# Optimization experiments

Measured on AMD Instinct MI355X. Metric: run time of the kernel, lower is better.

## Reference

```python
import jax, jax.numpy as jnp
import numpy as np

EPS = 1e-12  # matches torch F.normalize default eps

def _l2_normalize(x):
    # F.normalize: x / max(||x||, eps)
    n = jnp.linalg.norm(x, axis=-1, keepdims=True)
    return x / jnp.maximum(n, EPS)

def setup_inputs() -> dict:
    key = jax.random.key(0)
    k1, k2 = jax.random.split(key)
    sat = jax.random.normal(k1, (256, 64, 128), dtype=jnp.float32)   # [b, j, d]
    pano = jax.random.normal(k2, (64, 64, 128), dtype=jnp.float32)   # [a, i, d]
    return {"sat_embeddings_unnormalized": sat,
            "pano_embeddings_unnormalized": pano}

def reference(sat_embeddings_unnormalized, pano_embeddings_unnormalized):
    pano_n = _l2_normalize(pano_embeddings_unnormalized)  # [a, i, d]
    sat_n = _l2_normalize(sat_embeddings_unnormalized)    # [b, j, d]
    # similarity: [a, b, i, j]
    sim = jnp.einsum('aid,bjd->abij', pano_n, sat_n)
    # maxsim: max over sat tokens (j), sum over pano tokens (i) -> [a, b]
    return sim.max(axis=3).sum(axis=2)
```

## Files before the change

kernel.cpp:

```cpp
#include <hip/hip_runtime.h>
#include <hip/hip_bf16.h>


typedef __bf16 bf16x8 __attribute__((ext_vector_type(8)));
typedef float  f32x16 __attribute__((ext_vector_type(16)));
typedef unsigned int u32;

__device__ __forceinline__ void gload16(const void* g, void* l) {
    __builtin_amdgcn_global_load_lds((const __attribute__((address_space(1))) u32*)g,
                                     (__attribute__((address_space(3))) u32*)l, 16, 0, 0);
}

__device__ __forceinline__ unsigned short f2bf_rne(float x) {
    u32 u = __builtin_bit_cast(u32, x);
    return (unsigned short)((u + 0x7FFFu + ((u >> 16) & 1u)) >> 16);
}

__global__ __launch_bounds__(256) void normalize_all(
        const float* __restrict__ sat, const float* __restrict__ pano,
        unsigned short* __restrict__ satN, unsigned short* __restrict__ panoN) {
    int row  = blockIdx.x * 8 + (threadIdx.x >> 5);
    int lane = threadIdx.x & 31;
    const float* src;
    unsigned short* dst;
    if (row < 16384) { src = sat  + (size_t)row * 128;           dst = satN  + (size_t)row * 128; }
    else             { src = pano + (size_t)(row - 16384) * 128; dst = panoN + (size_t)(row - 16384) * 128; }
    const float4 v = *reinterpret_cast<const float4*>(src + lane * 4);
    float ss = v.x * v.x + v.y * v.y + v.z * v.z + v.w * v.w;
    #pragma unroll
    for (int m = 16; m >= 1; m >>= 1) ss += __shfl_xor(ss, m);
    float sc = 1.0f / fmaxf(sqrtf(ss), 1e-12f);
    ushort4 o;
    o.x = f2bf_rne(v.x * sc); o.y = f2bf_rne(v.y * sc);
    o.z = f2bf_rne(v.z * sc); o.w = f2bf_rne(v.w * sc);
    *reinterpret_cast<ushort4*>(dst + lane * 4) = o;
}

__global__ __launch_bounds__(512, 2) void maxsim_kernel(
        const unsigned short* __restrict__ satN,
        const unsigned short* __restrict__ panoN,
        float* __restrict__ out) {
    __shared__ unsigned short Plds[256 * 128];
    __shared__ unsigned short Slds[2][256 * 64];

    const int tid  = threadIdx.x;
    const int wid  = tid >> 6;
    const int lane = tid & 63;
    const int pt   = blockIdx.x >> 4;
    const int sg   = blockIdx.x & 15;

    const int wm = wid >> 2;
    const int wn = wid & 3;
    const int rl = lane & 31;
    const int hi = lane >> 5;

#define STAGE_SAT(stile, kh) do {                                              \
    const char* gb_ = (const char*)satN + ((size_t)(stile) * 256) * 256 + (kh) * 128; \
    char* lb_ = (char*)&Slds[kh][0];                                           \
    _Pragma("unroll")                                                          \
    for (int i_ = 0; i_ < 4; ++i_) {                                           \
        int P_ = (wid * 4 + i_) * 1024 + lane * 16;                            \
        int r_ = P_ >> 7;                                                      \
        int s_ = ((P_ >> 4) & 7) ^ (r_ & 7);                                   \
        gload16(gb_ + (size_t)r_ * 256 + s_ * 16, lb_ + P_);                   \
    } } while (0)

#define COMPUTE(kh) do {                                                       \
    const char* sb_ = (const char*)&Slds[kh][0];                               \
    const char* pb_ = (const char*)Plds;                                       \
    _Pragma("unroll")                                                          \
    for (int ks = 0; ks < 4; ++ks) {                                           \
        bf16x8 a_[4], b_[2];                                                   \
        _Pragma("unroll")                                                      \
        for (int m = 0; m < 4; ++m) {                                          \
            int row = wm * 128 + m * 32 + rl;                                  \
            a_[m] = *(const bf16x8*)(sb_ + row * 128 + ((((ks << 1) | hi) ^ (row & 7)) << 4)); \
        }                                                                      \
        _Pragma("unroll")                                                      \
        for (int n = 0; n < 2; ++n) {                                          \
            int row = wn * 64 + n * 32 + rl;                                   \
            b_[n] = *(const bf16x8*)(pb_ + row * 256 + ((((kh) * 8 + (ks << 1) + hi) ^ (row & 15)) << 4)); \
        }                                                                      \
        _Pragma("unroll")                                                      \
        for (int m = 0; m < 4; ++m)                                            \
            _Pragma("unroll")                                                  \
            for (int n = 0; n < 2; ++n)                                        \
                acc[m][n] = __builtin_amdgcn_mfma_f32_32x32x16_bf16(a_[m], b_[n], acc[m][n], 0, 0, 0); \
    } } while (0)

    {
        const char* pg = (const char*)(panoN + (size_t)pt * 256 * 128);
        char* pl = (char*)Plds;
        #pragma unroll
        for (int i = 0; i < 8; ++i) {
            int P   = (wid * 8 + i) * 1024 + lane * 16;
            int row = P >> 8;
            int ls  = ((P >> 4) & 15) ^ (row & 15);
            gload16(pg + row * 256 + ls * 16, pl + P);
        }
    }
    STAGE_SAT(sg * 4, 0);
    __syncthreads();

    for (int t = 0; t < 4; ++t) {
        const int st = sg * 4 + t;
        f32x16 acc[4][2] = {};

        STAGE_SAT(st, 1);
        __builtin_amdgcn_sched_barrier(0);
        COMPUTE(0);
        __syncthreads();

        if (t < 3) {
            STAGE_SAT(st + 1, 0);
            __builtin_amdgcn_sched_barrier(0);
        }
        COMPUTE(1);
        __syncthreads();

        #pragma unroll
        for (int jb = 0; jb < 2; ++jb) {
            float v0 = acc[2 * jb][0][0];
            float v1 = acc[2 * jb][1][0];
            #pragma unroll
            for (int m = 2 * jb; m <= 2 * jb + 1; ++m)
                #pragma unroll
                for (int q = 0; q < 16; ++q) {
                    if (m == 2 * jb && q == 0) continue;
                    v0 = fmaxf(v0, acc[m][0][q]);
                    v1 = fmaxf(v1, acc[m][1][q]);
                }
            v0 = fmaxf(v0, __shfl_xor(v0, 32));
            v1 = fmaxf(v1, __shfl_xor(v1, 32));
            float s = v0 + v1;
            #pragma unroll
            for (int d = 1; d <= 16; d <<= 1) s += __shfl_xor(s, d);
            if (lane == 0) {
                int a = pt * 4 + wn;
                int b = st * 4 + 2 * wm + jb;
                out[a * 256 + b] = s;
            }
        }
    }
#undef STAGE_SAT
#undef COMPUTE
}

extern "C" void kernel_launch(void* const* d_in, const int* in_sizes, int n_in,
                              void* d_out, int out_size, void* d_ws, size_t ws_size,
                              hipStream_t stream) {
    const float* sat  = (const float*)d_in[0];
    const float* pano = (const float*)d_in[1];
    float* out = (float*)d_out;

    unsigned short* panoN = (unsigned short*)d_ws;
    unsigned short* satN  = panoN + (size_t)4096 * 128;

    normalize_all<<<2560, 256, 0, stream>>>(sat, pano, satN, panoN);
    maxsim_kernel<<<256, 512, 0, stream>>>(satN, panoN, out);
}
```

Baseline: 27.78 us.

## Hold pano fragments in registers and shrink block tile to 128 pano rows

```diff
diff --git a/kernel.cpp b/kernel.cpp
--- a/kernel.cpp
+++ b/kernel.cpp
@@ -36,83 +36,80 @@
     *reinterpret_cast<ushort4*>(dst + lane * 4) = o;
 }
 
-__global__ __launch_bounds__(512, 2) void maxsim_kernel(
+__global__ __launch_bounds__(256, 2) void maxsim_kernel(
         const unsigned short* __restrict__ satN,
         const unsigned short* __restrict__ panoN,
         float* __restrict__ out) {
-    __shared__ unsigned short Plds[256 * 128];
     __shared__ unsigned short Slds[2][256 * 64];
 
     const int tid  = threadIdx.x;
     const int wid  = tid >> 6;
     const int lane = tid & 63;
-    const int pt   = blockIdx.x >> 4;
-    const int sg   = blockIdx.x & 15;
+    const int rl   = lane & 31;
+    const int hi   = lane >> 5;
 
-    const int wm = wid >> 2;
-    const int wn = wid & 3;
-    const int rl = lane & 31;
-    const int hi = lane >> 5;
+    const int bid = blockIdx.x;
+    const int swz = (bid & 7) * 64 + (bid >> 3);
+    const int jg  = swz >> 5;
+    const int it  = swz & 31;
 
-#define STAGE_SAT(stile, kh) do {                                              \
-    const char* gb_ = (const char*)satN + ((size_t)(stile) * 256) * 256 + (kh) * 128; \
+    const int wm = wid >> 1;
+    const int wn = wid & 1;
+
+    bf16x8 bfr[2][8];
+    {
+        const unsigned short* pb =
+            panoN + ((size_t)(it * 128 + wn * 64 + rl)) * 128 + hi * 8;
+        #pragma unroll
+        for (int n = 0; n < 2; ++n)
+            #pragma unroll
+            for (int kf = 0; kf < 8; ++kf)
+                bfr[n][kf] = *reinterpret_cast<const bf16x8*>(pb + n * 32 * 128 + kf * 16);
+    }
+
+#define STAGE(st, kh) do {                                                     \
+    const char* gb_ = (const char*)satN + (size_t)(st) * 65536 + (kh) * 128;   \
     char* lb_ = (char*)&Slds[kh][0];                                           \
     _Pragma("unroll")                                                          \
-    for (int i_ = 0; i_ < 4; ++i_) {                                           \
-        int P_ = (wid * 4 + i_) * 1024 + lane * 16;                            \
+    for (int i_ = 0; i_ < 8; ++i_) {                                           \
+        int P_ = (wid * 8 + i_) * 1024 + lane * 16;                            \
         int r_ = P_ >> 7;                                                      \
-        int s_ = ((P_ >> 4) & 7) ^ (r_ & 7);                                   \
-        gload16(gb_ + (size_t)r_ * 256 + s_ * 16, lb_ + P_);                   \
+        int g_ = ((P_ >> 4) & 7) ^ (r_ & 7);                                   \
+        gload16(gb_ + (size_t)r_ * 256 + g_ * 16, lb_ + P_);                   \
     } } while (0)
 
 #define COMPUTE(kh) do {                                                       \
     const char* sb_ = (const char*)&Slds[kh][0];                               \
-    const char* pb_ = (const char*)Plds;                                       \
     _Pragma("unroll")                                                          \
     for (int ks = 0; ks < 4; ++ks) {                                           \
-        bf16x8 a_[4], b_[2];                                                   \
+        bf16x8 a_[4];                                                          \
         _Pragma("unroll")                                                      \
         for (int m = 0; m < 4; ++m) {                                          \
             int row = wm * 128 + m * 32 + rl;                                  \
             a_[m] = *(const bf16x8*)(sb_ + row * 128 + ((((ks << 1) | hi) ^ (row & 7)) << 4)); \
         }                                                                      \
         _Pragma("unroll")                                                      \
-        for (int n = 0; n < 2; ++n) {                                          \
-            int row = wn * 64 + n * 32 + rl;                                   \
-            b_[n] = *(const bf16x8*)(pb_ + row * 256 + ((((kh) * 8 + (ks << 1) + hi) ^ (row & 15)) << 4)); \
-        }                                                                      \
-        _Pragma("unroll")                                                      \
         for (int m = 0; m < 4; ++m)                                            \
             _Pragma("unroll")                                                  \
             for (int n = 0; n < 2; ++n)                                        \
-                acc[m][n] = __builtin_amdgcn_mfma_f32_32x32x16_bf16(a_[m], b_[n], acc[m][n], 0, 0, 0); \
+                acc[m][n] = __builtin_amdgcn_mfma_f32_32x32x16_bf16(           \
+                    a_[m], bfr[n][(kh) * 4 + ks], acc[m][n], 0, 0, 0);         \
     } } while (0)
 
-    {
-        const char* pg = (const char*)(panoN + (size_t)pt * 256 * 128);
-        char* pl = (char*)Plds;
-        #pragma unroll
-        for (int i = 0; i < 8; ++i) {
-            int P   = (wid * 8 + i) * 1024 + lane * 16;
-            int row = P >> 8;
-            int ls  = ((P >> 4) & 15) ^ (row & 15);
-            gload16(pg + row * 256 + ls * 16, pl + P);
-        }
-    }
-    STAGE_SAT(sg * 4, 0);
+    STAGE(jg * 4, 0);
     __syncthreads();
 
     for (int t = 0; t < 4; ++t) {
-        const int st = sg * 4 + t;
+        const int st = jg * 4 + t;
         f32x16 acc[4][2] = {};
 
-        STAGE_SAT(st, 1);
+        STAGE(st, 1);
         __builtin_amdgcn_sched_barrier(0);
         COMPUTE(0);
         __syncthreads();
 
         if (t < 3) {
-            STAGE_SAT(st + 1, 0);
+            STAGE(st + 1, 0);
             __builtin_amdgcn_sched_barrier(0);
         }
         COMPUTE(1);
@@ -136,13 +133,13 @@
             #pragma unroll
             for (int d = 1; d <= 16; d <<= 1) s += __shfl_xor(s, d);
             if (lane == 0) {
-                int a = pt * 4 + wn;
-                int b = st * 4 + 2 * wm + jb;
+                int a = it * 2 + wn;
+                int b = st * 4 + wm * 2 + jb;
                 out[a * 256 + b] = s;
             }
         }
     }
-#undef STAGE_SAT
+#undef STAGE
 #undef COMPUTE
 }
 
@@ -157,5 +154,5 @@
     unsigned short* satN  = panoN + (size_t)4096 * 128;
 
     normalize_all<<<2560, 256, 0, stream>>>(sat, pano, satN, panoN);
-    maxsim_kernel<<<256, 512, 0, stream>>>(satN, panoN, out);
+    maxsim_kernel<<<512, 256, 0, stream>>>(satN, panoN, out);
 }
```

Measured after the change: 32.50 us. +17.0%, slower.
